# Kernel optimization log

Hardware: AMD Instinct MI355X
Metric: run time of the kernel (lower is better)

Reference implementation:

```python
import jax, jax.numpy as jnp
import numpy as np
from jax.scipy.special import logsumexp

V, H, NL, NH, DH, FF, S, B, T = 119547, 768, 12, 12, 64, 3072, 128, 16, 9
EPS = 1e-12  # BERT LayerNorm eps


def _ln(x, g, b):
    mu = jnp.mean(x, -1, keepdims=True)
    var = jnp.mean(jnp.square(x - mu), -1, keepdims=True)
    return g * (x - mu) * jax.lax.rsqrt(var + EPS) + b


def setup_inputs() -> dict:
    key = jax.random.key(0)
    ks = jax.random.split(key, 32)
    sc = 0.02
    n = lambda k, shp: jax.random.normal(k, shp, jnp.float32) * sc
    inp = {
        'ids': jax.random.randint(ks[0], (B, S), 0, V, dtype=jnp.int32),
        'mask': jnp.ones((B, S), jnp.int32),
        'token_type_ids': jnp.zeros((B, S), jnp.int32),
        'target_tags': jax.random.randint(ks[1], (B, S), 0, T, dtype=jnp.int32),
        # embeddings
        'word_emb': n(ks[2], (V, H)),
        'pos_emb': n(ks[3], (512, H)),
        'type_emb': n(ks[4], (2, H)),
        'emb_ln_g': jnp.ones((H,), jnp.float32),
        'emb_ln_b': jnp.zeros((H,), jnp.float32),
        # 12 stacked transformer layers
        'Wq': n(ks[5], (NL, H, H)), 'bq': jnp.zeros((NL, H), jnp.float32),
        'Wk': n(ks[6], (NL, H, H)), 'bk': jnp.zeros((NL, H), jnp.float32),
        'Wv': n(ks[7], (NL, H, H)), 'bv': jnp.zeros((NL, H), jnp.float32),
        'Wo': n(ks[8], (NL, H, H)), 'bo': jnp.zeros((NL, H), jnp.float32),
        'ln1_g': jnp.ones((NL, H), jnp.float32), 'ln1_b': jnp.zeros((NL, H), jnp.float32),
        'Wi': n(ks[9], (NL, H, FF)), 'bi': jnp.zeros((NL, FF), jnp.float32),
        'Wo2': n(ks[10], (NL, FF, H)), 'bo2': jnp.zeros((NL, H), jnp.float32),
        'ln2_g': jnp.ones((NL, H), jnp.float32), 'ln2_b': jnp.zeros((NL, H), jnp.float32),
        # tag projection
        'fc_w': n(ks[11], (H, T)), 'fc_b': jnp.zeros((T,), jnp.float32),
        # CRF params
        'crf_start': jax.random.uniform(ks[12], (T,), jnp.float32, -0.1, 0.1),
        'crf_end': jax.random.uniform(ks[13], (T,), jnp.float32, -0.1, 0.1),
        'crf_trans': jax.random.uniform(ks[14], (T, T), jnp.float32, -0.1, 0.1),
    }
    return inp


def _forward(ids, mask, token_type_ids, target_tags,
             word_emb, pos_emb, type_emb, emb_ln_g, emb_ln_b,
             Wq, bq, Wk, bk, Wv, bv, Wo, bo, ln1_g, ln1_b,
             Wi, bi, Wo2, bo2, ln2_g, ln2_b,
             fc_w, fc_b, crf_start, crf_end, crf_trans):
    maskf = mask.astype(jnp.float32)
    # --- BERT embeddings ---
    h = word_emb[ids] + pos_emb[None, :S] + type_emb[token_type_ids]
    h = _ln(h, emb_ln_g, emb_ln_b)
    attn_bias = (1.0 - maskf)[:, None, None, :] * -1e9  # [B,1,1,S]

    def block(h, p):
        wq, bq_, wk, bk_, wv, bv_, wo, bo_, g1, b1, wi, bi_, wo2, bo2_, g2, b2 = p
        q = (h @ wq + bq_).reshape(B, S, NH, DH)
        k = (h @ wk + bk_).reshape(B, S, NH, DH)
        v = (h @ wv + bv_).reshape(B, S, NH, DH)
        scores = jnp.einsum('bqnd,bknd->bnqk', q, k) / np.sqrt(DH) + attn_bias
        probs = jax.nn.softmax(scores, axis=-1)
        ctx = jnp.einsum('bnqk,bknd->bqnd', probs, v).reshape(B, S, H)
        h = _ln(h + ctx @ wo + bo_, g1, b1)
        ffn = jax.nn.gelu(h @ wi + bi_, approximate=False) @ wo2 + bo2_
        return _ln(h + ffn, g2, b2), None

    layer_stack = (Wq, bq, Wk, bk, Wv, bv, Wo, bo, ln1_g, ln1_b,
                   Wi, bi, Wo2, bo2, ln2_g, ln2_b)
    h, _ = jax.lax.scan(block, h, layer_stack)

    emissions = h @ fc_w + fc_b  # [B,S,T]

    # --- CRF log-likelihood (torchcrf semantics, reduction='mean') ---
    first_tags = target_tags[:, 0]
    emit = jnp.take_along_axis(emissions, target_tags[..., None].astype(jnp.int32), axis=2)[..., 0]  # [B,S]
    trans_sc = crf_trans[target_tags[:, :-1], target_tags[:, 1:]]  # [B,S-1]
    num = crf_start[first_tags] + emit[:, 0] + jnp.sum((trans_sc + emit[:, 1:]) * maskf[:, 1:], axis=1)
    last_idx = jnp.sum(mask, axis=1).astype(jnp.int32) - 1
    last_tags = jnp.take_along_axis(target_tags, last_idx[:, None], axis=1)[:, 0]
    num = num + crf_end[last_tags]

    alpha0 = crf_start[None, :] + emissions[:, 0]  # [B,T]

    def crf_step(alpha, xs):
        e_t, m_t = xs  # [B,T], [B]
        nxt = logsumexp(alpha[:, :, None] + crf_trans[None] + e_t[:, None, :], axis=1)
        return jnp.where(m_t[:, None], nxt, alpha), None

    alpha, _ = jax.lax.scan(crf_step, alpha0,
                            (jnp.swapaxes(emissions, 0, 1)[1:], mask.astype(bool).T[1:]))
    logZ = logsumexp(alpha + crf_end[None, :], axis=1)
    llh = num - logZ
    loss = -jnp.mean(llh)
    return emissions, loss


def reference(ids, mask, token_type_ids, target_tags,
              word_emb, pos_emb, type_emb, emb_ln_g, emb_ln_b,
              Wq, bq, Wk, bk, Wv, bv, Wo, bo, ln1_g, ln1_b,
              Wi, bi, Wo2, bo2, ln2_g, ln2_b,
              fc_w, fc_b, crf_start, crf_end, crf_trans):
    return _forward(ids, mask, token_type_ids, target_tags,
                    word_emb, pos_emb, type_emb, emb_ln_g, emb_ln_b,
                    Wq, bq, Wk, bk, Wv, bv, Wo, bo, ln1_g, ln1_b,
                    Wi, bi, Wo2, bo2, ln2_g, ln2_b,
                    fc_w, fc_b, crf_start, crf_end, crf_trans)
```

## Files before the change

### kernel.cpp

```cpp
#include <hip/hip_runtime.h>
#include <math.h>

#define NB   16
#define SS   128
#define HH   768
#define NHD  12
#define DHD  64
#define FFD  3072
#define NLAY 12
#define NT   9
#define TOK  (NB*SS)

typedef __attribute__((ext_vector_type(4))) float    f32x4;
typedef __attribute__((ext_vector_type(4))) _Float16 f16x4;
typedef __attribute__((ext_vector_type(8))) _Float16 f16x8;

__device__ __forceinline__ float wave_sum(float v) {
#pragma unroll
    for (int o = 32; o > 0; o >>= 1) v += __shfl_down(v, o, 64);
    return v;
}

__device__ __forceinline__ void split4(float4 v, f16x4& hv, f16x4& lv) {
    _Float16 h0 = (_Float16)v.x;
    _Float16 h1 = (_Float16)v.y;
    _Float16 h2 = (_Float16)v.z;
    _Float16 h3 = (_Float16)v.w;
    _Float16 l0 = (_Float16)((v.x - (float)h0) * 4096.0f);
    _Float16 l1 = (_Float16)((v.y - (float)h1) * 4096.0f);
    _Float16 l2 = (_Float16)((v.z - (float)h2) * 4096.0f);
    _Float16 l3 = (_Float16)((v.w - (float)h3) * 4096.0f);
    hv = (f16x4){h0, h1, h2, h3};
    lv = (f16x4){l0, l1, l2, l3};
}

__device__ __forceinline__ int lds_off(int row, int kbyte) {
    return (row << 6) + (kbyte ^ (((row >> 1) & 3) << 4));
}

__device__ __forceinline__ void gemm_core(
    const float* __restrict__ A, const float* __restrict__ W,
    const float* __restrict__ bias, float* __restrict__ C,
    int N, int K, int row0, int col0)
{
    __shared__ __align__(16) char lds[24576];
    char* aH = lds;
    char* aL = lds + 4096;
    char* bH = lds + 8192;
    char* bL = lds + 16384;

    const int tid  = threadIdx.x;
    const int lane = tid & 63;
    const int wid  = tid >> 6;
    const int wr   = wid >> 1;
    const int wc   = wid & 1;
    const int lrow = lane & 15;
    const int kby  = (lane >> 4) << 4;

    const int ar0 = tid >> 3;
    const int ar1 = ar0 + 32;
    const int ak  = (tid & 7) << 2;
    const int ak2 = ak << 1;
    const int bkb = tid >> 5;
    const int bn  = (tid & 31) << 2;
    const int kb2 = bkb << 3;

    const float* Ap0 = A + (size_t)(row0 + ar0) * K + ak;
    const float* Ap1 = A + (size_t)(row0 + ar1) * K + ak;
    const float* Wp  = W + (size_t)(bkb << 2) * N + col0 + bn;

    f32x4 acc1[2][4] = {};
    f32x4 acc2[2][4] = {};

    float4 av0 = *(const float4*)Ap0;
    float4 av1 = *(const float4*)Ap1;
    float4 w0  = *(const float4*)(Wp);
    float4 w1  = *(const float4*)(Wp + N);
    float4 w2  = *(const float4*)(Wp + 2 * (size_t)N);
    float4 w3  = *(const float4*)(Wp + 3 * (size_t)N);

    for (int k0 = 0; k0 < K; k0 += 32) {
        __syncthreads();
        {
            f16x4 hv, lv;
            split4(av0, hv, lv);
            *(f16x4*)(aH + lds_off(ar0, ak2)) = hv;
            *(f16x4*)(aL + lds_off(ar0, ak2)) = lv;
            split4(av1, hv, lv);
            *(f16x4*)(aH + lds_off(ar1, ak2)) = hv;
            *(f16x4*)(aL + lds_off(ar1, ak2)) = lv;
        }
        {
            f16x4 hv, lv;
            split4(make_float4(w0.x, w1.x, w2.x, w3.x), hv, lv);
            *(f16x4*)(bH + lds_off(bn + 0, kb2)) = hv;
            *(f16x4*)(bL + lds_off(bn + 0, kb2)) = lv;
            split4(make_float4(w0.y, w1.y, w2.y, w3.y), hv, lv);
            *(f16x4*)(bH + lds_off(bn + 1, kb2)) = hv;
            *(f16x4*)(bL + lds_off(bn + 1, kb2)) = lv;
            split4(make_float4(w0.z, w1.z, w2.z, w3.z), hv, lv);
            *(f16x4*)(bH + lds_off(bn + 2, kb2)) = hv;
            *(f16x4*)(bL + lds_off(bn + 2, kb2)) = lv;
            split4(make_float4(w0.w, w1.w, w2.w, w3.w), hv, lv);
            *(f16x4*)(bH + lds_off(bn + 3, kb2)) = hv;
            *(f16x4*)(bL + lds_off(bn + 3, kb2)) = lv;
        }
        __syncthreads();
        if (k0 + 32 < K) {
            av0 = *(const float4*)(Ap0 + k0 + 32);
            av1 = *(const float4*)(Ap1 + k0 + 32);
            const float* Wn = Wp + (size_t)(k0 + 32) * N;
            w0 = *(const float4*)(Wn);
            w1 = *(const float4*)(Wn + N);
            w2 = *(const float4*)(Wn + 2 * (size_t)N);
            w3 = *(const float4*)(Wn + 3 * (size_t)N);
        }
        f16x8 fAh[2], fAl[2], fBh[4], fBl[4];
#pragma unroll
        for (int i = 0; i < 2; i++) {
            int r = (wr << 5) + (i << 4) + lrow;
            int o = lds_off(r, kby);
            fAh[i] = *(const f16x8*)(aH + o);
            fAl[i] = *(const f16x8*)(aL + o);
        }
#pragma unroll
        for (int j = 0; j < 4; j++) {
            int n = (wc << 6) + (j << 4) + lrow;
            int o = lds_off(n, kby);
            fBh[j] = *(const f16x8*)(bH + o);
            fBl[j] = *(const f16x8*)(bL + o);
        }
#pragma unroll
        for (int i = 0; i < 2; i++)
#pragma unroll
            for (int j = 0; j < 4; j++) {
                acc1[i][j] = __builtin_amdgcn_mfma_f32_16x16x32_f16(fAh[i], fBh[j], acc1[i][j], 0, 0, 0);
                acc2[i][j] = __builtin_amdgcn_mfma_f32_16x16x32_f16(fAh[i], fBl[j], acc2[i][j], 0, 0, 0);
                acc2[i][j] = __builtin_amdgcn_mfma_f32_16x16x32_f16(fAl[i], fBh[j], acc2[i][j], 0, 0, 0);
            }
    }
    const int rb = row0 + (wr << 5) + ((lane >> 4) << 2);
    const int cb = col0 + (wc << 6) + lrow;
#pragma unroll
    for (int j = 0; j < 4; j++) {
        int c = cb + (j << 4);
        float bv = bias[c];
#pragma unroll
        for (int i = 0; i < 2; i++) {
            int r = rb + (i << 4);
            float* Cp = C + (size_t)r * N + c;
            Cp[0]             = acc1[i][j][0] + acc2[i][j][0] * 0.000244140625f + bv;
            Cp[(size_t)N]     = acc1[i][j][1] + acc2[i][j][1] * 0.000244140625f + bv;
            Cp[2 * (size_t)N] = acc1[i][j][2] + acc2[i][j][2] * 0.000244140625f + bv;
            Cp[3 * (size_t)N] = acc1[i][j][3] + acc2[i][j][3] * 0.000244140625f + bv;
        }
    }
}

__global__ __launch_bounds__(256) void gemm_k(
    const float* __restrict__ A, const float* __restrict__ W,
    const float* __restrict__ bias, float* __restrict__ C, int N, int K)
{
    gemm_core(A, W, bias, C, N, K, blockIdx.y * 64, blockIdx.x * 128);
}

__global__ __launch_bounds__(256) void qkv_k(
    const float* __restrict__ A,
    const float* __restrict__ Wq, const float* __restrict__ Wk, const float* __restrict__ Wv,
    const float* __restrict__ bq, const float* __restrict__ bk, const float* __restrict__ bv,
    float* __restrict__ Q, float* __restrict__ Ko, float* __restrict__ V, int Kd)
{
    int mat = blockIdx.x / 6;
    int cb  = blockIdx.x % 6;
    const float* W = (mat == 0) ? Wq : (mat == 1) ? Wk : Wv;
    const float* b = (mat == 0) ? bq : (mat == 1) ? bk : bv;
    float*       C = (mat == 0) ? Q  : (mat == 1) ? Ko : V;
    gemm_core(A, W, b, C, HH, Kd, blockIdx.y * 64, cb * 128);
}

__global__ __launch_bounds__(256) void embed_ln_k(
    const int* __restrict__ ids, const int* __restrict__ tt,
    const float* __restrict__ we, const float* __restrict__ pe,
    const float* __restrict__ te, const float* __restrict__ g,
    const float* __restrict__ bb, float* __restrict__ out)
{
    int tok = blockIdx.x;
    int s = tok % SS;
    int id = ids[tok];
    int ty = tt[tok];
    const float* wr = we + (size_t)id * HH;
    const float* pr = pe + (size_t)s * HH;
    const float* tr = te + (size_t)ty * HH;

    float x[3];
    float sum = 0.f;
#pragma unroll
    for (int i = 0; i < 3; i++) {
        int c = threadIdx.x + i * 256;
        float v = wr[c] + pr[c] + tr[c];
        x[i] = v; sum += v;
    }
    __shared__ float red[4];
    int lane = threadIdx.x & 63, wid = threadIdx.x >> 6;
    float t1 = wave_sum(sum);
    if (lane == 0) red[wid] = t1;
    __syncthreads();
    float mean = (red[0] + red[1] + red[2] + red[3]) * (1.0f / HH);
    __syncthreads();
    float sq = 0.f;
#pragma unroll
    for (int i = 0; i < 3; i++) { x[i] -= mean; sq += x[i] * x[i]; }
    float t2 = wave_sum(sq);
    if (lane == 0) red[wid] = t2;
    __syncthreads();
    float var = (red[0] + red[1] + red[2] + red[3]) * (1.0f / HH);
    float inv = rsqrtf(var + 1e-12f);
    float* o = out + (size_t)tok * HH;
#pragma unroll
    for (int i = 0; i < 3; i++) {
        int c = threadIdx.x + i * 256;
        o[c] = g[c] * x[i] * inv + bb[c];
    }
}

__global__ __launch_bounds__(256) void resln_k(
    float* __restrict__ h, const float* __restrict__ p,
    const float* __restrict__ g, const float* __restrict__ bb)
{
    int tok = blockIdx.x;
    float* hr = h + (size_t)tok * HH;
    const float* pr = p + (size_t)tok * HH;
    float x[3];
    float sum = 0.f;
#pragma unroll
    for (int i = 0; i < 3; i++) {
        int c = threadIdx.x + i * 256;
        float v = hr[c] + pr[c];
        x[i] = v; sum += v;
    }
    __shared__ float red[4];
    int lane = threadIdx.x & 63, wid = threadIdx.x >> 6;
    float t1 = wave_sum(sum);
    if (lane == 0) red[wid] = t1;
    __syncthreads();
    float mean = (red[0] + red[1] + red[2] + red[3]) * (1.0f / HH);
    __syncthreads();
    float sq = 0.f;
#pragma unroll
    for (int i = 0; i < 3; i++) { x[i] -= mean; sq += x[i] * x[i]; }
    float t2 = wave_sum(sq);
    if (lane == 0) red[wid] = t2;
    __syncthreads();
    float var = (red[0] + red[1] + red[2] + red[3]) * (1.0f / HH);
    float inv = rsqrtf(var + 1e-12f);
#pragma unroll
    for (int i = 0; i < 3; i++) {
        int c = threadIdx.x + i * 256;
        hr[c] = g[c] * x[i] * inv + bb[c];
    }
}

__global__ __launch_bounds__(256) void attn_scores_k(
    const float* __restrict__ Qb, const float* __restrict__ Kb,
    const int* __restrict__ mask, float* __restrict__ Sc)
{
    int bh = blockIdx.x;
    int b = bh / NHD, hh = bh % NHD;
    __shared__ float Ks[SS][DHD + 1];
    for (int i = threadIdx.x; i < SS * DHD; i += 256) {
        int k = i >> 6, d = i & 63;
        Ks[k][d] = Kb[(size_t)(b * SS + k) * HH + hh * DHD + d];
    }
    __syncthreads();
    int kk = threadIdx.x & 127;
    int qh = threadIdx.x >> 7;
    float biasv = (1.0f - (float)mask[b * SS + kk]) * -1e9f;
    for (int q = qh; q < SS; q += 2) {
        const float* Qr = Qb + (size_t)(b * SS + q) * HH + hh * DHD;
        float acc = 0.f;
#pragma unroll 8
        for (int d = 0; d < DHD; d++) acc += Qr[d] * Ks[kk][d];
        Sc[((size_t)bh * SS + q) * SS + kk] = acc * 0.125f + biasv;
    }
}

__global__ __launch_bounds__(64) void softmax_k(float* __restrict__ Sc)
{
    size_t row = blockIdx.x;
    float* p = Sc + row * SS;
    int t = threadIdx.x;
    float a = p[t], b = p[t + 64];
    float mx = fmaxf(a, b);
#pragma unroll
    for (int o = 32; o > 0; o >>= 1) mx = fmaxf(mx, __shfl_down(mx, o, 64));
    mx = __shfl(mx, 0, 64);
    float ea = expf(a - mx), eb = expf(b - mx);
    float sm = ea + eb;
#pragma unroll
    for (int o = 32; o > 0; o >>= 1) sm += __shfl_down(sm, o, 64);
    sm = __shfl(sm, 0, 64);
    float inv = 1.0f / sm;
    p[t] = ea * inv;
    p[t + 64] = eb * inv;
}

__global__ __launch_bounds__(256) void attn_ctx_k(
    const float* __restrict__ Sc, const float* __restrict__ Vb,
    float* __restrict__ Cb)
{
    int bh = blockIdx.x;
    int b = bh / NHD, hh = bh % NHD;
    __shared__ float Vs[SS][DHD];
    for (int i = threadIdx.x; i < SS * DHD; i += 256) {
        int k = i >> 6, d = i & 63;
        Vs[k][d] = Vb[(size_t)(b * SS + k) * HH + hh * DHD + d];
    }
    __syncthreads();
    int d = threadIdx.x & 63;
    int qg = threadIdx.x >> 6;
    for (int q = qg; q < SS; q += 4) {
        const float* P = Sc + ((size_t)bh * SS + q) * SS;
        float acc = 0.f;
#pragma unroll 8
        for (int k = 0; k < SS; k++) acc += P[k] * Vs[k][d];
        Cb[(size_t)(b * SS + q) * HH + hh * DHD + d] = acc;
    }
}

__global__ __launch_bounds__(256) void gelu_k(float* __restrict__ x, int n4)
{
    int i = blockIdx.x * 256 + threadIdx.x;
    if (i < n4) {
        float4 v = ((float4*)x)[i];
        v.x = 0.5f * v.x * (1.f + erff(v.x * 0.70710678118654752f));
        v.y = 0.5f * v.y * (1.f + erff(v.y * 0.70710678118654752f));
        v.z = 0.5f * v.z * (1.f + erff(v.z * 0.70710678118654752f));
        v.w = 0.5f * v.w * (1.f + erff(v.w * 0.70710678118654752f));
        ((float4*)x)[i] = v;
    }
}

__global__ __launch_bounds__(64) void emissions_k(
    const float* __restrict__ h, const float* __restrict__ fcw,
    const float* __restrict__ fcb, float* __restrict__ em)
{
    int tok = blockIdx.x;
    const float* hr = h + (size_t)tok * HH;
    float acc[NT];
#pragma unroll
    for (int t = 0; t < NT; t++) acc[t] = 0.f;
    for (int c = threadIdx.x; c < HH; c += 64) {
        float x = hr[c];
#pragma unroll
        for (int t = 0; t < NT; t++) acc[t] += x * fcw[c * NT + t];
    }
#pragma unroll
    for (int t = 0; t < NT; t++) {
        float v = wave_sum(acc[t]);
        if (threadIdx.x == 0) em[(size_t)tok * NT + t] = v + fcb[t];
    }
}

__global__ __launch_bounds__(64) void crf_k(
    const float* __restrict__ em, const int* __restrict__ tags,
    const int* __restrict__ mask, const float* __restrict__ startv,
    const float* __restrict__ endv, const float* __restrict__ trans,
    float* __restrict__ llh)
{
    int b = blockIdx.x;
    const float* E = em + (size_t)b * SS * NT;
    __shared__ float alpha[NT];
    __shared__ float nalpha[NT];
    int j = threadIdx.x;
    if (j < NT) alpha[j] = startv[j] + E[j];
    __syncthreads();
    for (int t = 1; t < SS; t++) {
        if (j < NT) {
            int m = mask[b * SS + t];
            float mx = -1e30f;
#pragma unroll
            for (int i = 0; i < NT; i++) mx = fmaxf(mx, alpha[i] + trans[i * NT + j]);
            float sm = 0.f;
#pragma unroll
            for (int i = 0; i < NT; i++) sm += expf(alpha[i] + trans[i * NT + j] - mx);
            float nx = mx + logf(sm) + E[t * NT + j];
            nalpha[j] = m ? nx : alpha[j];
        }
        __syncthreads();
        if (j < NT) alpha[j] = nalpha[j];
        __syncthreads();
    }
    if (j == 0) {
        float mx = -1e30f;
        for (int i = 0; i < NT; i++) mx = fmaxf(mx, alpha[i] + endv[i]);
        float sm = 0.f;
        for (int i = 0; i < NT; i++) sm += expf(alpha[i] + endv[i] - mx);
        float logZ = mx + logf(sm);

        const int* tg = tags + b * SS;
        float num = startv[tg[0]] + E[tg[0]];
        for (int t = 1; t < SS; t++) {
            float msk = (float)mask[b * SS + t];
            num += (trans[tg[t - 1] * NT + tg[t]] + E[t * NT + tg[t]]) * msk;
        }
        int cnt = 0;
        for (int t = 0; t < SS; t++) cnt += mask[b * SS + t];
        num += endv[tg[cnt - 1]];
        llh[b] = num - logZ;
    }
}

__global__ __launch_bounds__(64) void loss_k(const float* __restrict__ llh, float* __restrict__ out)
{
    if (threadIdx.x == 0) {
        float s = 0.f;
        for (int b = 0; b < NB; b++) s += llh[b];
        out[0] = -s / NB;
    }
}

extern "C" void kernel_launch(void* const* d_in, const int* in_sizes, int n_in,
                              void* d_out, int out_size, void* d_ws, size_t ws_size,
                              hipStream_t stream)
{
    const int* ids  = (const int*)d_in[0];
    const int* mask = (const int*)d_in[1];
    const int* tt   = (const int*)d_in[2];
    const int* tags = (const int*)d_in[3];
    const float* wemb = (const float*)d_in[4];
    const float* pemb = (const float*)d_in[5];
    const float* temb = (const float*)d_in[6];
    const float* elg  = (const float*)d_in[7];
    const float* elb  = (const float*)d_in[8];
    const float* Wq = (const float*)d_in[9];
    const float* bq = (const float*)d_in[10];
    const float* Wk = (const float*)d_in[11];
    const float* bk = (const float*)d_in[12];
    const float* Wv = (const float*)d_in[13];
    const float* bv = (const float*)d_in[14];
    const float* Wo = (const float*)d_in[15];
    const float* bo = (const float*)d_in[16];
    const float* g1 = (const float*)d_in[17];
    const float* b1 = (const float*)d_in[18];
    const float* Wi = (const float*)d_in[19];
    const float* bi = (const float*)d_in[20];
    const float* Wo2 = (const float*)d_in[21];
    const float* bo2 = (const float*)d_in[22];
    const float* g2 = (const float*)d_in[23];
    const float* b2 = (const float*)d_in[24];
    const float* fcw = (const float*)d_in[25];
    const float* fcb = (const float*)d_in[26];
    const float* cst = (const float*)d_in[27];
    const float* cen = (const float*)d_in[28];
    const float* ctr = (const float*)d_in[29];

    float* ws = (float*)d_ws;
    const size_t TH = (size_t)TOK * HH;
    float* h  = ws;
    float* qb = h + TH;
    float* kb = qb + TH;
    float* vb = kb + TH;
    float* ob = vb + TH;
    float* sc = ob + TH;
    float* ff = sc + (size_t)NB * NHD * SS * SS;
    float* llh = ff + (size_t)TOK * FFD;

    float* emis = (float*)d_out;
    float* loss = emis + (size_t)TOK * NT;

    embed_ln_k<<<TOK, 256, 0, stream>>>(ids, tt, wemb, pemb, temb, elg, elb, h);

    dim3 gQKV(3 * (HH / 128), TOK / 64);
    dim3 gH(HH / 128, TOK / 64);
    dim3 gF(FFD / 128, TOK / 64);

    for (int l = 0; l < NLAY; l++) {
        const float* wql = Wq + (size_t)l * HH * HH;  const float* bql = bq + (size_t)l * HH;
        const float* wkl = Wk + (size_t)l * HH * HH;  const float* bkl = bk + (size_t)l * HH;
        const float* wvl = Wv + (size_t)l * HH * HH;  const float* bvl = bv + (size_t)l * HH;
        const float* wol = Wo + (size_t)l * HH * HH;  const float* bol = bo + (size_t)l * HH;
        const float* g1l = g1 + (size_t)l * HH;       const float* b1l = b1 + (size_t)l * HH;
        const float* wil = Wi + (size_t)l * HH * FFD; const float* bil = bi + (size_t)l * FFD;
        const float* w2l = Wo2 + (size_t)l * FFD * HH; const float* b2l_ = bo2 + (size_t)l * HH;
        const float* g2l = g2 + (size_t)l * HH;       const float* b2l = b2 + (size_t)l * HH;

        qkv_k<<<gQKV, 256, 0, stream>>>(h, wql, wkl, wvl, bql, bkl, bvl, qb, kb, vb, HH);
        attn_scores_k<<<NB * NHD, 256, 0, stream>>>(qb, kb, mask, sc);
        softmax_k<<<NB * NHD * SS, 64, 0, stream>>>(sc);
        attn_ctx_k<<<NB * NHD, 256, 0, stream>>>(sc, vb, ob);
        gemm_k<<<gH, 256, 0, stream>>>(ob, wol, bol, qb, HH, HH);
        resln_k<<<TOK, 256, 0, stream>>>(h, qb, g1l, b1l);
        gemm_k<<<gF, 256, 0, stream>>>(h, wil, bil, ff, FFD, HH);
        gelu_k<<<(TOK * FFD / 4 + 255) / 256, 256, 0, stream>>>(ff, TOK * FFD / 4);
        gemm_k<<<gH, 256, 0, stream>>>(ff, w2l, b2l_, qb, HH, FFD);
        resln_k<<<TOK, 256, 0, stream>>>(h, qb, g2l, b2l);
    }

    emissions_k<<<TOK, 64, 0, stream>>>(h, fcw, fcb, emis);
    crf_k<<<NB, 64, 0, stream>>>(emis, tags, mask, cst, cen, ctr, llh);
    loss_k<<<1, 64, 0, stream>>>(llh, loss);
}
```

Measured before the change: 6.193 ms.

## Pre-split weights and activations into fp16 hi/lo pairs and fuse GELU into GEMM

Adds a conversion kernel that transposes each weight matrix and splits it into fp16 high and low parts. Producer kernels (embedding LN, residual LN, attention context) now write fp16 hi/lo copies of their activations, so the GEMM main loop only copies f16x8 vectors into LDS instead of splitting fp32 values each tile. GELU moves into the FFN-up GEMM epilogue, which writes split fp16 output and removes the separate GELU pass over the fp32 buffer. The weight conversion runs on every call and reads and writes all layer weights, and the workspace grows to hold the converted copies.

```diff
diff --git a/kernel.cpp b/kernel.cpp
--- a/kernel.cpp
+++ b/kernel.cpp
@@ -12,7 +12,6 @@
 #define TOK  (NB*SS)
 
 typedef __attribute__((ext_vector_type(4))) float    f32x4;
-typedef __attribute__((ext_vector_type(4))) _Float16 f16x4;
 typedef __attribute__((ext_vector_type(8))) _Float16 f16x8;
 
 __device__ __forceinline__ float wave_sum(float v) {
@@ -21,26 +20,48 @@
     return v;
 }
 
-__device__ __forceinline__ void split4(float4 v, f16x4& hv, f16x4& lv) {
-    _Float16 h0 = (_Float16)v.x;
-    _Float16 h1 = (_Float16)v.y;
-    _Float16 h2 = (_Float16)v.z;
-    _Float16 h3 = (_Float16)v.w;
-    _Float16 l0 = (_Float16)((v.x - (float)h0) * 4096.0f);
-    _Float16 l1 = (_Float16)((v.y - (float)h1) * 4096.0f);
-    _Float16 l2 = (_Float16)((v.z - (float)h2) * 4096.0f);
-    _Float16 l3 = (_Float16)((v.w - (float)h3) * 4096.0f);
-    hv = (f16x4){h0, h1, h2, h3};
-    lv = (f16x4){l0, l1, l2, l3};
-}
-
 __device__ __forceinline__ int lds_off(int row, int kbyte) {
     return (row << 6) + (kbyte ^ (((row >> 1) & 3) << 4));
 }
 
+__global__ __launch_bounds__(256) void wconv_k(
+    const float* __restrict__ W, _Float16* __restrict__ WtH,
+    _Float16* __restrict__ WtL, int K, int N)
+{
+    __shared__ _Float16 tH[32][33];
+    __shared__ _Float16 tL[32][33];
+    const size_t lstr = (size_t)K * N;
+    const float* Wl = W + lstr * blockIdx.z;
+    _Float16* oH = WtH + lstr * blockIdx.z;
+    _Float16* oL = WtL + lstr * blockIdx.z;
+    int n0 = blockIdx.x * 32, k0 = blockIdx.y * 32;
+    int tn = threadIdx.x & 31;
+    int tk = threadIdx.x >> 5;
+#pragma unroll
+    for (int i = 0; i < 4; i++) {
+        int k = tk + i * 8;
+        float v = Wl[(size_t)(k0 + k) * N + n0 + tn];
+        _Float16 hh = (_Float16)v;
+        tH[k][tn] = hh;
+        tL[k][tn] = (_Float16)((v - (float)hh) * 4096.0f);
+    }
+    __syncthreads();
+    int wk = threadIdx.x & 31;
+    int wn = threadIdx.x >> 5;
+#pragma unroll
+    for (int i = 0; i < 4; i++) {
+        int n = wn + i * 8;
+        oH[(size_t)(n0 + n) * K + k0 + wk] = tH[wk][n];
+        oL[(size_t)(n0 + n) * K + k0 + wk] = tL[wk][n];
+    }
+}
+
+template<int EPI>
 __device__ __forceinline__ void gemm_core(
-    const float* __restrict__ A, const float* __restrict__ W,
+    const _Float16* __restrict__ aHp, const _Float16* __restrict__ aLp,
+    const _Float16* __restrict__ bHp, const _Float16* __restrict__ bLp,
     const float* __restrict__ bias, float* __restrict__ C,
+    _Float16* __restrict__ gH, _Float16* __restrict__ gL,
     int N, int K, int row0, int col0)
 {
     __shared__ __align__(16) char lds[24576];
@@ -57,63 +78,43 @@
     const int lrow = lane & 15;
     const int kby  = (lane >> 4) << 4;
 
-    const int ar0 = tid >> 3;
-    const int ar1 = ar0 + 32;
-    const int ak  = (tid & 7) << 2;
-    const int ak2 = ak << 1;
-    const int bkb = tid >> 5;
-    const int bn  = (tid & 31) << 2;
-    const int kb2 = bkb << 3;
-
-    const float* Ap0 = A + (size_t)(row0 + ar0) * K + ak;
-    const float* Ap1 = A + (size_t)(row0 + ar1) * K + ak;
-    const float* Wp  = W + (size_t)(bkb << 2) * N + col0 + bn;
+    const int srow  = tid >> 2;
+    const int sslot = (tid & 3) << 4;
+    const int sk    = (tid & 3) << 3;
+
+    const _Float16* ApH  = aHp + (size_t)(row0 + srow) * K + sk;
+    const _Float16* ApL  = aLp + (size_t)(row0 + srow) * K + sk;
+    const _Float16* BpH0 = bHp + (size_t)(col0 + srow) * K + sk;
+    const _Float16* BpL0 = bLp + (size_t)(col0 + srow) * K + sk;
+    const _Float16* BpH1 = bHp + (size_t)(col0 + 64 + srow) * K + sk;
+    const _Float16* BpL1 = bLp + (size_t)(col0 + 64 + srow) * K + sk;
 
     f32x4 acc1[2][4] = {};
     f32x4 acc2[2][4] = {};
 
-    float4 av0 = *(const float4*)Ap0;
-    float4 av1 = *(const float4*)Ap1;
-    float4 w0  = *(const float4*)(Wp);
-    float4 w1  = *(const float4*)(Wp + N);
-    float4 w2  = *(const float4*)(Wp + 2 * (size_t)N);
-    float4 w3  = *(const float4*)(Wp + 3 * (size_t)N);
+    f16x8 ra_h = *(const f16x8*)ApH;
+    f16x8 ra_l = *(const f16x8*)ApL;
+    f16x8 rb0h = *(const f16x8*)BpH0;
+    f16x8 rb0l = *(const f16x8*)BpL0;
+    f16x8 rb1h = *(const f16x8*)BpH1;
+    f16x8 rb1l = *(const f16x8*)BpL1;
 
     for (int k0 = 0; k0 < K; k0 += 32) {
         __syncthreads();
-        {
-            f16x4 hv, lv;
-            split4(av0, hv, lv);
-            *(f16x4*)(aH + lds_off(ar0, ak2)) = hv;
-            *(f16x4*)(aL + lds_off(ar0, ak2)) = lv;
-            split4(av1, hv, lv);
-            *(f16x4*)(aH + lds_off(ar1, ak2)) = hv;
-            *(f16x4*)(aL + lds_off(ar1, ak2)) = lv;
-        }
-        {
-            f16x4 hv, lv;
-            split4(make_float4(w0.x, w1.x, w2.x, w3.x), hv, lv);
-            *(f16x4*)(bH + lds_off(bn + 0, kb2)) = hv;
-            *(f16x4*)(bL + lds_off(bn + 0, kb2)) = lv;
-            split4(make_float4(w0.y, w1.y, w2.y, w3.y), hv, lv);
-            *(f16x4*)(bH + lds_off(bn + 1, kb2)) = hv;
-            *(f16x4*)(bL + lds_off(bn + 1, kb2)) = lv;
-            split4(make_float4(w0.z, w1.z, w2.z, w3.z), hv, lv);
-            *(f16x4*)(bH + lds_off(bn + 2, kb2)) = hv;
-            *(f16x4*)(bL + lds_off(bn + 2, kb2)) = lv;
-            split4(make_float4(w0.w, w1.w, w2.w, w3.w), hv, lv);
-            *(f16x4*)(bH + lds_off(bn + 3, kb2)) = hv;
-            *(f16x4*)(bL + lds_off(bn + 3, kb2)) = lv;
-        }
+        *(f16x8*)(aH + lds_off(srow, sslot))      = ra_h;
+        *(f16x8*)(aL + lds_off(srow, sslot))      = ra_l;
+        *(f16x8*)(bH + lds_off(srow, sslot))      = rb0h;
+        *(f16x8*)(bL + lds_off(srow, sslot))      = rb0l;
+        *(f16x8*)(bH + lds_off(64 + srow, sslot)) = rb1h;
+        *(f16x8*)(bL + lds_off(64 + srow, sslot)) = rb1l;
         __syncthreads();
         if (k0 + 32 < K) {
-            av0 = *(const float4*)(Ap0 + k0 + 32);
-            av1 = *(const float4*)(Ap1 + k0 + 32);
-            const float* Wn = Wp + (size_t)(k0 + 32) * N;
-            w0 = *(const float4*)(Wn);
-            w1 = *(const float4*)(Wn + N);
-            w2 = *(const float4*)(Wn + 2 * (size_t)N);
-            w3 = *(const float4*)(Wn + 3 * (size_t)N);
+            ra_h = *(const f16x8*)(ApH  + k0 + 32);
+            ra_l = *(const f16x8*)(ApL  + k0 + 32);
+            rb0h = *(const f16x8*)(BpH0 + k0 + 32);
+            rb0l = *(const f16x8*)(BpL0 + k0 + 32);
+            rb1h = *(const f16x8*)(BpH1 + k0 + 32);
+            rb1l = *(const f16x8*)(BpL1 + k0 + 32);
         }
         f16x8 fAh[2], fAl[2], fBh[4], fBl[4];
 #pragma unroll
@@ -148,41 +149,58 @@
 #pragma unroll
         for (int i = 0; i < 2; i++) {
             int r = rb + (i << 4);
-            float* Cp = C + (size_t)r * N + c;
-            Cp[0]             = acc1[i][j][0] + acc2[i][j][0] * 0.000244140625f + bv;
-            Cp[(size_t)N]     = acc1[i][j][1] + acc2[i][j][1] * 0.000244140625f + bv;
-            Cp[2 * (size_t)N] = acc1[i][j][2] + acc2[i][j][2] * 0.000244140625f + bv;
-            Cp[3 * (size_t)N] = acc1[i][j][3] + acc2[i][j][3] * 0.000244140625f + bv;
+#pragma unroll
+            for (int t = 0; t < 4; t++) {
+                float v = acc1[i][j][t] + acc2[i][j][t] * 0.000244140625f + bv;
+                if (EPI == 0) {
+                    C[(size_t)(r + t) * N + c] = v;
+                } else {
+                    v = 0.5f * v * (1.f + erff(v * 0.70710678118654752f));
+                    _Float16 vh = (_Float16)v;
+                    gH[(size_t)(r + t) * N + c] = vh;
+                    gL[(size_t)(r + t) * N + c] = (_Float16)((v - (float)vh) * 4096.0f);
+                }
+            }
         }
     }
 }
 
+template<int EPI>
 __global__ __launch_bounds__(256) void gemm_k(
-    const float* __restrict__ A, const float* __restrict__ W,
-    const float* __restrict__ bias, float* __restrict__ C, int N, int K)
-{
-    gemm_core(A, W, bias, C, N, K, blockIdx.y * 64, blockIdx.x * 128);
+    const _Float16* __restrict__ aH, const _Float16* __restrict__ aL,
+    const _Float16* __restrict__ bH, const _Float16* __restrict__ bL,
+    const float* __restrict__ bias, float* __restrict__ C,
+    _Float16* __restrict__ gH, _Float16* __restrict__ gL, int N, int K)
+{
+    gemm_core<EPI>(aH, aL, bH, bL, bias, C, gH, gL, N, K,
+                   blockIdx.y * 64, blockIdx.x * 128);
 }
 
 __global__ __launch_bounds__(256) void qkv_k(
-    const float* __restrict__ A,
-    const float* __restrict__ Wq, const float* __restrict__ Wk, const float* __restrict__ Wv,
-    const float* __restrict__ bq, const float* __restrict__ bk, const float* __restrict__ bv,
-    float* __restrict__ Q, float* __restrict__ Ko, float* __restrict__ V, int Kd)
+    const _Float16* __restrict__ aH, const _Float16* __restrict__ aL,
+    const _Float16* __restrict__ qH, const _Float16* __restrict__ qL,
+    const _Float16* __restrict__ kH, const _Float16* __restrict__ kL,
+    const _Float16* __restrict__ vH, const _Float16* __restrict__ vL,
+    const float* __restrict__ bq, const float* __restrict__ bk,
+    const float* __restrict__ bv,
+    float* __restrict__ Q, float* __restrict__ Ko, float* __restrict__ V)
 {
     int mat = blockIdx.x / 6;
     int cb  = blockIdx.x % 6;
-    const float* W = (mat == 0) ? Wq : (mat == 1) ? Wk : Wv;
-    const float* b = (mat == 0) ? bq : (mat == 1) ? bk : bv;
-    float*       C = (mat == 0) ? Q  : (mat == 1) ? Ko : V;
-    gemm_core(A, W, b, C, HH, Kd, blockIdx.y * 64, cb * 128);
+    const _Float16* bH = (mat == 0) ? qH : (mat == 1) ? kH : vH;
+    const _Float16* bL = (mat == 0) ? qL : (mat == 1) ? kL : vL;
+    const float* bias  = (mat == 0) ? bq : (mat == 1) ? bk : bv;
+    float* C           = (mat == 0) ? Q  : (mat == 1) ? Ko : V;
+    gemm_core<0>(aH, aL, bH, bL, bias, C, nullptr, nullptr, HH, HH,
+                 blockIdx.y * 64, cb * 128);
 }
 
 __global__ __launch_bounds__(256) void embed_ln_k(
     const int* __restrict__ ids, const int* __restrict__ tt,
     const float* __restrict__ we, const float* __restrict__ pe,
     const float* __restrict__ te, const float* __restrict__ g,
-    const float* __restrict__ bb, float* __restrict__ out)
+    const float* __restrict__ bb, float* __restrict__ out,
+    _Float16* __restrict__ pH, _Float16* __restrict__ pL)
 {
     int tok = blockIdx.x;
     int s = tok % SS;
@@ -216,16 +234,23 @@
     float var = (red[0] + red[1] + red[2] + red[3]) * (1.0f / HH);
     float inv = rsqrtf(var + 1e-12f);
     float* o = out + (size_t)tok * HH;
+    _Float16* oh = pH + (size_t)tok * HH;
+    _Float16* ol = pL + (size_t)tok * HH;
 #pragma unroll
     for (int i = 0; i < 3; i++) {
         int c = threadIdx.x + i * 256;
-        o[c] = g[c] * x[i] * inv + bb[c];
+        float v = g[c] * x[i] * inv + bb[c];
+        o[c] = v;
+        _Float16 vh = (_Float16)v;
+        oh[c] = vh;
+        ol[c] = (_Float16)((v - (float)vh) * 4096.0f);
     }
 }
 
 __global__ __launch_bounds__(256) void resln_k(
     float* __restrict__ h, const float* __restrict__ p,
-    const float* __restrict__ g, const float* __restrict__ bb)
+    const float* __restrict__ g, const float* __restrict__ bb,
+    _Float16* __restrict__ pH, _Float16* __restrict__ pL)
 {
     int tok = blockIdx.x;
     float* hr = h + (size_t)tok * HH;
@@ -253,10 +278,16 @@
     __syncthreads();
     float var = (red[0] + red[1] + red[2] + red[3]) * (1.0f / HH);
     float inv = rsqrtf(var + 1e-12f);
+    _Float16* oh = pH + (size_t)tok * HH;
+    _Float16* ol = pL + (size_t)tok * HH;
 #pragma unroll
     for (int i = 0; i < 3; i++) {
         int c = threadIdx.x + i * 256;
-        hr[c] = g[c] * x[i] * inv + bb[c];
+        float v = g[c] * x[i] * inv + bb[c];
+        hr[c] = v;
+        _Float16 vh = (_Float16)v;
+        oh[c] = vh;
+        ol[c] = (_Float16)((v - (float)vh) * 4096.0f);
     }
 }
 
@@ -306,7 +337,7 @@
 
 __global__ __launch_bounds__(256) void attn_ctx_k(
     const float* __restrict__ Sc, const float* __restrict__ Vb,
-    float* __restrict__ Cb)
+    _Float16* __restrict__ oPH, _Float16* __restrict__ oPL)
 {
     int bh = blockIdx.x;
     int b = bh / NHD, hh = bh % NHD;
@@ -323,20 +354,10 @@
         float acc = 0.f;
 #pragma unroll 8
         for (int k = 0; k < SS; k++) acc += P[k] * Vs[k][d];
-        Cb[(size_t)(b * SS + q) * HH + hh * DHD + d] = acc;
-    }
-}
-
-__global__ __launch_bounds__(256) void gelu_k(float* __restrict__ x, int n4)
-{
-    int i = blockIdx.x * 256 + threadIdx.x;
-    if (i < n4) {
-        float4 v = ((float4*)x)[i];
-        v.x = 0.5f * v.x * (1.f + erff(v.x * 0.70710678118654752f));
-        v.y = 0.5f * v.y * (1.f + erff(v.y * 0.70710678118654752f));
-        v.z = 0.5f * v.z * (1.f + erff(v.z * 0.70710678118654752f));
-        v.w = 0.5f * v.w * (1.f + erff(v.w * 0.70710678118654752f));
-        ((float4*)x)[i] = v;
+        size_t o = (size_t)(b * SS + q) * HH + hh * DHD + d;
+        _Float16 ch = (_Float16)acc;
+        oPH[o] = ch;
+        oPL[o] = (_Float16)((acc - (float)ch) * 4096.0f);
     }
 }
 
@@ -456,44 +477,69 @@
 
     float* ws = (float*)d_ws;
     const size_t TH = (size_t)TOK * HH;
+    const size_t TF = (size_t)TOK * FFD;
     float* h  = ws;
     float* qb = h + TH;
     float* kb = qb + TH;
     float* vb = kb + TH;
-    float* ob = vb + TH;
-    float* sc = ob + TH;
-    float* ff = sc + (size_t)NB * NHD * SS * SS;
-    float* llh = ff + (size_t)TOK * FFD;
+    float* sc = vb + TH;
+    float* llh = sc + (size_t)NB * NHD * SS * SS;
+
+    _Float16* fp = (_Float16*)(llh + 64);
+    _Float16* hPH = fp; fp += TH;   _Float16* hPL = fp; fp += TH;
+    _Float16* oPH = fp; fp += TH;   _Float16* oPL = fp; fp += TH;
+    _Float16* fPH = fp; fp += TF;   _Float16* fPL = fp; fp += TF;
+    const size_t WH2 = (size_t)NLAY * HH * HH;
+    const size_t WHF = (size_t)NLAY * HH * FFD;
+    _Float16* WqH = fp; fp += WH2;  _Float16* WqL = fp; fp += WH2;
+    _Float16* WkH = fp; fp += WH2;  _Float16* WkL = fp; fp += WH2;
+    _Float16* WvH = fp; fp += WH2;  _Float16* WvL = fp; fp += WH2;
+    _Float16* WoH = fp; fp += WH2;  _Float16* WoL = fp; fp += WH2;
+    _Float16* WiH = fp; fp += WHF;  _Float16* WiL = fp; fp += WHF;
+    _Float16* W2H = fp; fp += WHF;  _Float16* W2L = fp; fp += WHF;
 
     float* emis = (float*)d_out;
     float* loss = emis + (size_t)TOK * NT;
 
-    embed_ln_k<<<TOK, 256, 0, stream>>>(ids, tt, wemb, pemb, temb, elg, elb, h);
-
-    dim3 gQKV(3 * (HH / 128), TOK / 64);
+    wconv_k<<<dim3(HH / 32, HH / 32, NLAY), 256, 0, stream>>>(Wq, WqH, WqL, HH, HH);
+    wconv_k<<<dim3(HH / 32, HH / 32, NLAY), 256, 0, stream>>>(Wk, WkH, WkL, HH, HH);
+    wconv_k<<<dim3(HH / 32, HH / 32, NLAY), 256, 0, stream>>>(Wv, WvH, WvL, HH, HH);
+    wconv_k<<<dim3(HH / 32, HH / 32, NLAY), 256, 0, stream>>>(Wo, WoH, WoL, HH, HH);
+    wconv_k<<<dim3(FFD / 32, HH / 32, NLAY), 256, 0, stream>>>(Wi, WiH, WiL, HH, FFD);
+    wconv_k<<<dim3(HH / 32, FFD / 32, NLAY), 256, 0, stream>>>(Wo2, W2H, W2L, FFD, HH);
+
+    embed_ln_k<<<TOK, 256, 0, stream>>>(ids, tt, wemb, pemb, temb, elg, elb, h, hPH, hPL);
+
+    dim3 gQKV(18, TOK / 64);
     dim3 gH(HH / 128, TOK / 64);
     dim3 gF(FFD / 128, TOK / 64);
 
     for (int l = 0; l < NLAY; l++) {
-        const float* wql = Wq + (size_t)l * HH * HH;  const float* bql = bq + (size_t)l * HH;
-        const float* wkl = Wk + (size_t)l * HH * HH;  const float* bkl = bk + (size_t)l * HH;
-        const float* wvl = Wv + (size_t)l * HH * HH;  const float* bvl = bv + (size_t)l * HH;
-        const float* wol = Wo + (size_t)l * HH * HH;  const float* bol = bo + (size_t)l * HH;
-        const float* g1l = g1 + (size_t)l * HH;       const float* b1l = b1 + (size_t)l * HH;
-        const float* wil = Wi + (size_t)l * HH * FFD; const float* bil = bi + (size_t)l * FFD;
-        const float* w2l = Wo2 + (size_t)l * FFD * HH; const float* b2l_ = bo2 + (size_t)l * HH;
-        const float* g2l = g2 + (size_t)l * HH;       const float* b2l = b2 + (size_t)l * HH;
-
-        qkv_k<<<gQKV, 256, 0, stream>>>(h, wql, wkl, wvl, bql, bkl, bvl, qb, kb, vb, HH);
+        const size_t w2 = (size_t)l * HH * HH;
+        const size_t wf = (size_t)l * HH * FFD;
+        const float* bql = bq + (size_t)l * HH;
+        const float* bkl = bk + (size_t)l * HH;
+        const float* bvl = bv + (size_t)l * HH;
+        const float* bol = bo + (size_t)l * HH;
+        const float* g1l = g1 + (size_t)l * HH;  const float* b1l = b1 + (size_t)l * HH;
+        const float* bil = bi + (size_t)l * FFD;
+        const float* b2l_ = bo2 + (size_t)l * HH;
+        const float* g2l = g2 + (size_t)l * HH;  const float* b2l = b2 + (size_t)l * HH;
+
+        qkv_k<<<gQKV, 256, 0, stream>>>(hPH, hPL,
+            WqH + w2, WqL + w2, WkH + w2, WkL + w2, WvH + w2, WvL + w2,
+            bql, bkl, bvl, qb, kb, vb);
         attn_scores_k<<<NB * NHD, 256, 0, stream>>>(qb, kb, mask, sc);
         softmax_k<<<NB * NHD * SS, 64, 0, stream>>>(sc);
-        attn_ctx_k<<<NB * NHD, 256, 0, stream>>>(sc, vb, ob);
-        gemm_k<<<gH, 256, 0, stream>>>(ob, wol, bol, qb, HH, HH);
-        resln_k<<<TOK, 256, 0, stream>>>(h, qb, g1l, b1l);
-        gemm_k<<<gF, 256, 0, stream>>>(h, wil, bil, ff, FFD, HH);
-        gelu_k<<<(TOK * FFD / 4 + 255) / 256, 256, 0, stream>>>(ff, TOK * FFD / 4);
-        gemm_k<<<gH, 256, 0, stream>>>(ff, w2l, b2l_, qb, HH, FFD);
-        resln_k<<<TOK, 256, 0, stream>>>(h, qb, g2l, b2l);
+        attn_ctx_k<<<NB * NHD, 256, 0, stream>>>(sc, vb, oPH, oPL);
+        gemm_k<0><<<gH, 256, 0, stream>>>(oPH, oPL, WoH + w2, WoL + w2,
+            bol, qb, nullptr, nullptr, HH, HH);
+        resln_k<<<TOK, 256, 0, stream>>>(h, qb, g1l, b1l, hPH, hPL);
+        gemm_k<1><<<gF, 256, 0, stream>>>(hPH, hPL, WiH + wf, WiL + wf,
+            bil, nullptr, fPH, fPL, FFD, HH);
+        gemm_k<0><<<gH, 256, 0, stream>>>(fPH, fPL, W2H + wf, W2L + wf,
+            b2l_, qb, nullptr, nullptr, HH, FFD);
+        resln_k<<<TOK, 256, 0, stream>>>(h, qb, g2l, b2l, hPH, hPL);
     }
 
     emissions_k<<<TOK, 64, 0, stream>>>(h, fcw, fcb, emis);
```

After: 5.057 ms. -18.4%, faster.
